# Optimization experiments

Measured on AMD Instinct MI355X. Metric: run time of the kernel, lower is better.

Reference implementation:

```python
import jax, jax.numpy as jnp
import numpy as np

N_NODES = 100000
N_EDGES = 1200000
N_GRAPHS = 1024
IN_DIM, HIDDEN, OUT_DIM = 4, 64, 2
BN_EPS = 1e-5


def setup_inputs() -> dict:
    key = jax.random.key(0)
    ks = jax.random.split(key, 12)
    x = jax.random.normal(ks[0], (N_NODES, IN_DIM), dtype=jnp.float32)
    edge_index = jax.random.randint(ks[1], (2, N_EDGES), 0, N_NODES, dtype=jnp.int64)
    batch = jnp.sort(jax.random.randint(ks[2], (N_NODES,), 0, N_GRAPHS, dtype=jnp.int64))
    s = 1.0 / np.sqrt(HIDDEN)
    return {
        "x": x,
        "edge_index": edge_index,
        "batch": batch,
        "W_enc": jax.random.normal(ks[3], (IN_DIM, HIDDEN), dtype=jnp.float32) * 0.5,
        "b_enc": jnp.zeros((HIDDEN,), dtype=jnp.float32),
        "bn_gamma": jnp.ones((HIDDEN,), dtype=jnp.float32),
        "bn_beta": jnp.zeros((HIDDEN,), dtype=jnp.float32),
        "bn_mean": jax.random.normal(ks[4], (HIDDEN,), dtype=jnp.float32) * 0.1,
        "bn_var": jax.random.uniform(ks[5], (HIDDEN,), dtype=jnp.float32, minval=0.5, maxval=1.5),
        "W_gcn": jax.random.normal(ks[6], (HIDDEN, HIDDEN), dtype=jnp.float32) * s,
        "b_gcn": jnp.zeros((HIDDEN,), dtype=jnp.float32),
        "W_cls1": jax.random.normal(ks[7], (HIDDEN, HIDDEN), dtype=jnp.float32) * s,
        "b_cls1": jnp.zeros((HIDDEN,), dtype=jnp.float32),
        "W_cls2": jax.random.normal(ks[8], (HIDDEN, OUT_DIM), dtype=jnp.float32) * s,
        "b_cls2": jnp.zeros((OUT_DIM,), dtype=jnp.float32),
    }


def reference(x, edge_index, batch, W_enc, b_enc, bn_gamma, bn_beta, bn_mean, bn_var,
              W_gcn, b_gcn, W_cls1, b_cls1, W_cls2, b_cls2):
    n = x.shape[0]
    # Encoder: Linear -> ReLU -> Dropout(eval=identity) -> BatchNorm1d (running stats)
    h = jnp.maximum(x @ W_enc + b_enc, 0.0)
    h = (h - bn_mean) * jax.lax.rsqrt(bn_var + BN_EPS) * bn_gamma + bn_beta
    # GCNConv (PyG): add self-loops, symmetric deg^{-1/2} normalization
    loop = jnp.arange(n, dtype=edge_index.dtype)
    src = jnp.concatenate([edge_index[0], loop])  # [E+N]
    dst = jnp.concatenate([edge_index[1], loop])
    deg = jnp.zeros((n,), dtype=h.dtype).at[dst].add(1.0)
    dis = jnp.where(deg > 0, jax.lax.rsqrt(jnp.maximum(deg, 1.0)), 0.0)
    norm = dis[src] * dis[dst]  # [E+N]
    hw = h @ W_gcn  # [N, H]
    msg = hw[src] * norm[:, None]  # gather + scale, [E+N, H]
    agg = jax.ops.segment_sum(msg, dst, num_segments=n) + b_gcn
    agg = jnp.maximum(agg, 0.0)  # .relu()
    # global_mean_pool over graphs
    sums = jax.ops.segment_sum(agg, batch, num_segments=N_GRAPHS)  # [G, H]
    cnts = jax.ops.segment_sum(jnp.ones((n,), dtype=agg.dtype), batch, num_segments=N_GRAPHS)
    gm = sums / jnp.maximum(cnts, 1.0)[:, None]
    # Classifier: Linear -> ReLU -> Dropout(eval) -> Linear
    out = jnp.maximum(gm @ W_cls1 + b_cls1, 0.0) @ W_cls2 + b_cls2
    return out
```

## Files before the change

### kernel.cpp

```cpp
#include <hip/hip_runtime.h>

#define N_NODES  100000
#define N_EDGES  1200000
#define N_GRAPHS 1024

#define BUCK_SHIFT 10
#define BUCK_NODES 1024
#define NBUCK 98
#define FBLK  512
#define CHUNK ((N_EDGES + FBLK - 1) / FBLK)

__device__ __forceinline__ unsigned short f2bf(float f) {
  unsigned u = __float_as_uint(f);
  return (unsigned short)((u + 0x7fffu + ((u >> 16) & 1u)) >> 16);
}
__device__ __forceinline__ float bf2f(unsigned short b) {
  return __uint_as_float(((unsigned)b) << 16);
}

__global__ __launch_bounds__(256) void k_cnt(const int* __restrict__ ei,
                                             int* __restrict__ cnt,
                                             float* __restrict__ gsum) {
  __shared__ int h[NBUCK];
  int t = threadIdx.x;
  for (int i = t; i < NBUCK; i += 256) h[i] = 0;
  int gi = blockIdx.x * 256 + t;
  if (gi < N_GRAPHS * 64) gsum[gi] = 0.f;
  __syncthreads();
  int start = blockIdx.x * CHUNK, end = min(start + CHUNK, N_EDGES);
  for (int e = start + t; e < end; e += 256)
    atomicAdd(&h[ei[N_EDGES + e] >> BUCK_SHIFT], 1);
  __syncthreads();
  for (int b = t; b < NBUCK; b += 256)
    cnt[b * FBLK + blockIdx.x] = h[b];
}

__global__ __launch_bounds__(256) void k_colscan(int* __restrict__ cnt,
                                                 int* __restrict__ tot) {
  __shared__ int wsum[4];
  int b = blockIdx.x, t = threadIdx.x;
  int v0 = cnt[b * FBLK + 2 * t], v1 = cnt[b * FBLK + 2 * t + 1];
  int a = v0 + v1;
  int lane = t & 63, w = t >> 6;
  int incl = a;
  #pragma unroll
  for (int off = 1; off < 64; off <<= 1) {
    int y = __shfl_up(incl, off);
    if (lane >= off) incl += y;
  }
  if (lane == 63) wsum[w] = incl;
  __syncthreads();
  if (t == 0) {
    int s = 0;
    #pragma unroll
    for (int i = 0; i < 4; ++i) { int x = wsum[i]; wsum[i] = s; s += x; }
    tot[b] = s;
  }
  __syncthreads();
  int excl = wsum[w] + incl - a;
  cnt[b * FBLK + 2 * t] = excl;
  cnt[b * FBLK + 2 * t + 1] = excl + v0;
}

__global__ void k_base(const int* __restrict__ tot, int* __restrict__ base) {
  __shared__ int s[128];
  int t = threadIdx.x;
  int v = (t < NBUCK) ? tot[t] : 0;
  s[t] = v;
  __syncthreads();
  for (int off = 1; off < 128; off <<= 1) {
    int x = (t >= off) ? s[t - off] : 0;
    __syncthreads();
    s[t] += x;
    __syncthreads();
  }
  if (t < NBUCK) base[t] = s[t] - v;
  if (t == 0) base[NBUCK] = N_EDGES;
}

__global__ __launch_bounds__(256) void k_fill(const int* __restrict__ ei,
                                              const int* __restrict__ cnt,
                                              const int* __restrict__ base,
                                              int* __restrict__ binned) {
  __shared__ int cur[NBUCK];
  int t = threadIdx.x, blk = blockIdx.x;
  for (int b = t; b < NBUCK; b += 256) cur[b] = base[b] + cnt[b * FBLK + blk];
  __syncthreads();
  int start = blk * CHUNK, end = min(start + CHUNK, N_EDGES);
  for (int e = start + t; e < end; e += 256) {
    int src = ei[e];
    int dst = ei[N_EDGES + e];
    int b = dst >> BUCK_SHIFT;
    int p = atomicAdd(&cur[b], 1);
    binned[p] = src | ((dst & (BUCK_NODES - 1)) << 17);
  }
}

__global__ __launch_bounds__(1024) void k_csr(const int* __restrict__ base,
                                              const int* __restrict__ binned,
                                              int* __restrict__ csr,
                                              int* __restrict__ row_start,
                                              float* __restrict__ dis) {
  __shared__ int hist[BUCK_NODES];
  __shared__ int wsum[16];
  int t = threadIdx.x;
  int blk = blockIdx.x;
  int b0 = base[blk];
  int nE = base[blk + 1] - b0;
  int node0 = blk << BUCK_SHIFT;
  int nNodes = min(BUCK_NODES, N_NODES - node0);
  hist[t] = 0;
  __syncthreads();
  for (int i = t; i < nE; i += 1024)
    atomicAdd(&hist[(unsigned)binned[b0 + i] >> 17], 1);
  __syncthreads();
  int v = hist[t];
  int lane = t & 63, w = t >> 6;
  int incl = v;
  #pragma unroll
  for (int off = 1; off < 64; off <<= 1) {
    int y = __shfl_up(incl, off);
    if (lane >= off) incl += y;
  }
  if (lane == 63) wsum[w] = incl;
  __syncthreads();
  if (t == 0) {
    int s = 0;
    #pragma unroll
    for (int i = 0; i < 16; ++i) { int x = wsum[i]; wsum[i] = s; s += x; }
  }
  __syncthreads();
  int excl = wsum[w] + incl - v;
  hist[t] = excl;
  if (t < nNodes) {
    row_start[node0 + t] = b0 + excl;
    dis[node0 + t] = rsqrtf((float)(v + 1));
  }
  if (t == 0 && blk == NBUCK - 1) row_start[N_NODES] = N_EDGES;
  __syncthreads();
  for (int i = t; i < nE; i += 1024) {
    int vv = binned[b0 + i];
    int d = (unsigned)vv >> 17;
    int p = atomicAdd(&hist[d], 1);
    csr[b0 + p] = vv & 0x1FFFF;
  }
}

__global__ __launch_bounds__(256) void k_enc(
    const float* __restrict__ x,
    const float* __restrict__ Wenc, const float* __restrict__ benc,
    const float* __restrict__ gamma, const float* __restrict__ beta,
    const float* __restrict__ mean,  const float* __restrict__ var,
    const float* __restrict__ Wgcn,  const float* __restrict__ dis,
    unsigned short* __restrict__ hws) {
  int lane = threadIdx.x & 63;
  int wv = (blockIdx.x * 256 + threadIdx.x) >> 6;
  float be = benc[lane];
  float sc = gamma[lane] * rsqrtf(var[lane] + 1e-5f);
  float mu = mean[lane], bt = beta[lane];
  float w0 = Wenc[lane], w1 = Wenc[64 + lane], w2 = Wenc[128 + lane], w3 = Wenc[192 + lane];
  float wreg[64];
  #pragma unroll
  for (int k = 0; k < 64; ++k) wreg[k] = Wgcn[k * 64 + lane];
  int n0 = wv * 16;
  for (int i = 0; i < 16; ++i) {
    int n = n0 + i;
    float4 xv = ((const float4*)x)[n];
    float h = fmaf(xv.w, w3, fmaf(xv.z, w2, fmaf(xv.y, w1, fmaf(xv.x, w0, be))));
    h = fmaxf(h, 0.f);
    float hbn = (h - mu) * sc + bt;
    int hb = __float_as_int(hbn);
    float a0 = 0.f, a1 = 0.f, a2 = 0.f, a3 = 0.f;
    #pragma unroll
    for (int k = 0; k < 64; k += 4) {
      a0 = fmaf(__int_as_float(__builtin_amdgcn_readlane(hb, k)),     wreg[k],     a0);
      a1 = fmaf(__int_as_float(__builtin_amdgcn_readlane(hb, k + 1)), wreg[k + 1], a1);
      a2 = fmaf(__int_as_float(__builtin_amdgcn_readlane(hb, k + 2)), wreg[k + 2], a2);
      a3 = fmaf(__int_as_float(__builtin_amdgcn_readlane(hb, k + 3)), wreg[k + 3], a3);
    }
    float acc = ((a0 + a1) + (a2 + a3)) * dis[n];
    hws[(size_t)n * 64 + lane] = f2bf(acc);
  }
}

__global__ __launch_bounds__(256) void k_gather(
    const int* __restrict__ row_start, const int* __restrict__ csr,
    const float* __restrict__ dis, const unsigned short* __restrict__ hws,
    const int* __restrict__ batch, const float* __restrict__ bgcn,
    float* __restrict__ gsum) {
  int lane = threadIdx.x & 63;
  int wv = blockIdx.x * 4 + (threadIdx.x >> 6);
  int nb = wv * 4;
  if (nb >= N_NODES) return;
  float bias = bgcn[lane];
  float vout[4];
  int gid[4];
  #pragma unroll
  for (int k = 0; k < 4; ++k) {
    int n = nb + k;
    int st = row_start[n], en = row_start[n + 1];
    float dn = dis[n];
    float a0 = 0.f, a1 = 0.f, a2 = 0.f, a3 = 0.f;
    for (int c = st; c < en; c += 64) {
      int idx = c + lane;
      int sj = (idx < en) ? csr[idx] : 0;
      int m = min(64, en - c);
      int j = 0;
      for (; j + 8 <= m; j += 8) {
        int s0 = __shfl(sj, j),     s1 = __shfl(sj, j + 1);
        int s2 = __shfl(sj, j + 2), s3 = __shfl(sj, j + 3);
        int s4 = __shfl(sj, j + 4), s5 = __shfl(sj, j + 5);
        int s6 = __shfl(sj, j + 6), s7 = __shfl(sj, j + 7);
        float r0 = bf2f(hws[(size_t)s0 * 64 + lane]);
        float r1 = bf2f(hws[(size_t)s1 * 64 + lane]);
        float r2 = bf2f(hws[(size_t)s2 * 64 + lane]);
        float r3 = bf2f(hws[(size_t)s3 * 64 + lane]);
        float r4 = bf2f(hws[(size_t)s4 * 64 + lane]);
        float r5 = bf2f(hws[(size_t)s5 * 64 + lane]);
        float r6 = bf2f(hws[(size_t)s6 * 64 + lane]);
        float r7 = bf2f(hws[(size_t)s7 * 64 + lane]);
        a0 += r0; a1 += r1; a2 += r2; a3 += r3;
        a0 += r4; a1 += r5; a2 += r6; a3 += r7;
      }
      for (; j < m; ++j) {
        int s = __shfl(sj, j);
        a0 += bf2f(hws[(size_t)s * 64 + lane]);
      }
    }
    float self = bf2f(hws[(size_t)n * 64 + lane]);
    vout[k] = fmaxf(dn * (((a0 + a1) + (a2 + a3)) + self) + bias, 0.f);
    gid[k] = batch[n];
  }
  float vs = vout[0];
  int cg = gid[0];
  #pragma unroll
  for (int k = 1; k < 4; ++k) {
    if (gid[k] == cg) vs += vout[k];
    else {
      atomicAdd(&gsum[cg * 64 + lane], vs);
      vs = vout[k]; cg = gid[k];
    }
  }
  atomicAdd(&gsum[cg * 64 + lane], vs);
}

__global__ void k_cls(const float* __restrict__ gsum, const int* __restrict__ batch,
                      const float* __restrict__ W1, const float* __restrict__ b1,
                      const float* __restrict__ W2, const float* __restrict__ b2,
                      float* __restrict__ out) {
  __shared__ float gm[64];
  __shared__ int cntS;
  int j = threadIdx.x;
  int g = blockIdx.x;
  if (j == 0) {
    int lo = 0, hi = N_NODES;
    while (lo < hi) { int mid = (lo + hi) >> 1; if (batch[mid] < g) lo = mid + 1; else hi = mid; }
    int lo2 = lo, hi2 = N_NODES;
    while (lo2 < hi2) { int mid = (lo2 + hi2) >> 1; if (batch[mid] < g + 1) lo2 = mid + 1; else hi2 = mid; }
    cntS = lo2 - lo;
  }
  __syncthreads();
  float denom = fmaxf((float)cntS, 1.0f);
  gm[j] = gsum[g * 64 + j] / denom;
  __syncthreads();
  float hid = b1[j];
  #pragma unroll
  for (int k = 0; k < 64; ++k) hid += gm[k] * W1[k * 64 + j];
  hid = fmaxf(hid, 0.f);
  float o0 = hid * W2[j * 2 + 0];
  float o1 = hid * W2[j * 2 + 1];
  #pragma unroll
  for (int off = 32; off > 0; off >>= 1) {
    o0 += __shfl_down(o0, off);
    o1 += __shfl_down(o1, off);
  }
  if (j == 0) {
    out[g * 2 + 0] = o0 + b2[0];
    out[g * 2 + 1] = o1 + b2[1];
  }
}

extern "C" void kernel_launch(void* const* d_in, const int* in_sizes, int n_in,
                              void* d_out, int out_size, void* d_ws, size_t ws_size,
                              hipStream_t stream) {
  const float* x     = (const float*)d_in[0];
  const int*   ei    = (const int*)d_in[1];
  const int*   batch = (const int*)d_in[2];
  const float* Wenc  = (const float*)d_in[3];
  const float* benc  = (const float*)d_in[4];
  const float* gamma = (const float*)d_in[5];
  const float* beta  = (const float*)d_in[6];
  const float* mean  = (const float*)d_in[7];
  const float* var   = (const float*)d_in[8];
  const float* Wgcn  = (const float*)d_in[9];
  const float* bgcn  = (const float*)d_in[10];
  const float* W1    = (const float*)d_in[11];
  const float* b1    = (const float*)d_in[12];
  const float* W2    = (const float*)d_in[13];
  const float* b2    = (const float*)d_in[14];
  float* out = (float*)d_out;

  char* ws = (char*)d_ws;
  float*          gsum      = (float*)ws;          ws += (size_t)N_GRAPHS * 64 * 4;
  int*            cnt       = (int*)ws;            ws += (size_t)NBUCK * FBLK * 4;
  int*            tot       = (int*)ws;            ws += 128 * 4;
  int*            basep     = (int*)ws;            ws += 128 * 4;
  int*            binned    = (int*)ws;            ws += (size_t)N_EDGES * 4;
  int*            csr       = (int*)ws;            ws += (size_t)N_EDGES * 4;
  int*            row_start = (int*)ws;            ws += (size_t)(N_NODES + 32) * 4;
  float*          dis       = (float*)ws;          ws += (size_t)N_NODES * 4;
  unsigned short* hws       = (unsigned short*)ws; ws += (size_t)N_NODES * 64 * 2;

  k_cnt<<<FBLK, 256, 0, stream>>>(ei, cnt, gsum);
  k_colscan<<<NBUCK, 256, 0, stream>>>(cnt, tot);
  k_base<<<1, 128, 0, stream>>>(tot, basep);
  k_fill<<<FBLK, 256, 0, stream>>>(ei, cnt, basep, binned);
  k_csr<<<NBUCK, 1024, 0, stream>>>(basep, binned, csr, row_start, dis);
  k_enc<<<(N_NODES / 16 + 3) / 4, 256, 0, stream>>>(x, Wenc, benc, gamma, beta, mean, var,
                                                    Wgcn, dis, hws);
  k_gather<<<(N_NODES / 16), 256, 0, stream>>>(row_start, csr, dis, hws, batch, bgcn, gsum);
  k_cls<<<N_GRAPHS, 64, 0, stream>>>(gsum, batch, W1, b1, W2, b2, out);
}
```

Baseline: 200.5 us.

## Fold bucket base scan into fill and CSR kernels; reshape gather launch

```diff
diff --git a/kernel.cpp b/kernel.cpp
--- a/kernel.cpp
+++ b/kernel.cpp
@@ -62,29 +62,20 @@
   cnt[b * FBLK + 2 * t + 1] = excl + v0;
 }
 
-__global__ void k_base(const int* __restrict__ tot, int* __restrict__ base) {
-  __shared__ int s[128];
-  int t = threadIdx.x;
-  int v = (t < NBUCK) ? tot[t] : 0;
-  s[t] = v;
-  __syncthreads();
-  for (int off = 1; off < 128; off <<= 1) {
-    int x = (t >= off) ? s[t - off] : 0;
-    __syncthreads();
-    s[t] += x;
-    __syncthreads();
-  }
-  if (t < NBUCK) base[t] = s[t] - v;
-  if (t == 0) base[NBUCK] = N_EDGES;
-}
-
 __global__ __launch_bounds__(256) void k_fill(const int* __restrict__ ei,
                                               const int* __restrict__ cnt,
-                                              const int* __restrict__ base,
+                                              const int* __restrict__ tot,
                                               int* __restrict__ binned) {
+  __shared__ int totS[NBUCK];
   __shared__ int cur[NBUCK];
   int t = threadIdx.x, blk = blockIdx.x;
-  for (int b = t; b < NBUCK; b += 256) cur[b] = base[b] + cnt[b * FBLK + blk];
+  if (t < NBUCK) totS[t] = tot[t];
+  __syncthreads();
+  if (t < NBUCK) {
+    int s = 0;
+    for (int i = 0; i < t; ++i) s += totS[i];
+    cur[t] = s + cnt[t * FBLK + blk];
+  }
   __syncthreads();
   int start = blk * CHUNK, end = min(start + CHUNK, N_EDGES);
   for (int e = start + t; e < end; e += 256) {
@@ -96,26 +87,38 @@
   }
 }
 
-__global__ __launch_bounds__(1024) void k_csr(const int* __restrict__ base,
+__global__ __launch_bounds__(1024) void k_csr(const int* __restrict__ tot,
                                               const int* __restrict__ binned,
                                               int* __restrict__ csr,
                                               int* __restrict__ row_start,
                                               float* __restrict__ dis) {
   __shared__ int hist[BUCK_NODES];
   __shared__ int wsum[16];
+  __shared__ int b0S;
   int t = threadIdx.x;
   int blk = blockIdx.x;
-  int b0 = base[blk];
-  int nE = base[blk + 1] - b0;
+  int lane = t & 63, w = t >> 6;
+  int pv = (t < blk) ? tot[t] : 0;
+  #pragma unroll
+  for (int off = 32; off > 0; off >>= 1) pv += __shfl_down(pv, off);
+  if (lane == 0) wsum[w] = pv;
+  hist[t] = 0;
+  __syncthreads();
+  if (t == 0) {
+    int s = 0;
+    #pragma unroll
+    for (int i = 0; i < 16; ++i) s += wsum[i];
+    b0S = s;
+  }
+  __syncthreads();
+  int b0 = b0S;
+  int nE = tot[blk];
   int node0 = blk << BUCK_SHIFT;
   int nNodes = min(BUCK_NODES, N_NODES - node0);
-  hist[t] = 0;
-  __syncthreads();
   for (int i = t; i < nE; i += 1024)
     atomicAdd(&hist[(unsigned)binned[b0 + i] >> 17], 1);
   __syncthreads();
   int v = hist[t];
-  int lane = t & 63, w = t >> 6;
   int incl = v;
   #pragma unroll
   for (int off = 1; off < 64; off <<= 1) {
@@ -183,15 +186,13 @@
   }
 }
 
-__global__ __launch_bounds__(256) void k_gather(
+__global__ __launch_bounds__(64) void k_gather(
     const int* __restrict__ row_start, const int* __restrict__ csr,
     const float* __restrict__ dis, const unsigned short* __restrict__ hws,
     const int* __restrict__ batch, const float* __restrict__ bgcn,
     float* __restrict__ gsum) {
-  int lane = threadIdx.x & 63;
-  int wv = blockIdx.x * 4 + (threadIdx.x >> 6);
-  int nb = wv * 4;
-  if (nb >= N_NODES) return;
+  int lane = threadIdx.x;
+  int nb = blockIdx.x * 4;
   float bias = bgcn[lane];
   float vout[4];
   int gid[4];
@@ -202,28 +203,21 @@
     float dn = dis[n];
     float a0 = 0.f, a1 = 0.f, a2 = 0.f, a3 = 0.f;
     for (int c = st; c < en; c += 64) {
-      int idx = c + lane;
-      int sj = (idx < en) ? csr[idx] : 0;
       int m = min(64, en - c);
+      int chunk = (c + lane < en) ? csr[c + lane] : 0;
       int j = 0;
-      for (; j + 8 <= m; j += 8) {
-        int s0 = __shfl(sj, j),     s1 = __shfl(sj, j + 1);
-        int s2 = __shfl(sj, j + 2), s3 = __shfl(sj, j + 3);
-        int s4 = __shfl(sj, j + 4), s5 = __shfl(sj, j + 5);
-        int s6 = __shfl(sj, j + 6), s7 = __shfl(sj, j + 7);
-        float r0 = bf2f(hws[(size_t)s0 * 64 + lane]);
-        float r1 = bf2f(hws[(size_t)s1 * 64 + lane]);
-        float r2 = bf2f(hws[(size_t)s2 * 64 + lane]);
-        float r3 = bf2f(hws[(size_t)s3 * 64 + lane]);
-        float r4 = bf2f(hws[(size_t)s4 * 64 + lane]);
-        float r5 = bf2f(hws[(size_t)s5 * 64 + lane]);
-        float r6 = bf2f(hws[(size_t)s6 * 64 + lane]);
-        float r7 = bf2f(hws[(size_t)s7 * 64 + lane]);
-        a0 += r0; a1 += r1; a2 += r2; a3 += r3;
-        a0 += r4; a1 += r5; a2 += r6; a3 += r7;
+      for (; j + 4 <= m; j += 4) {
+        int s0 = __builtin_amdgcn_readlane(chunk, j);
+        int s1 = __builtin_amdgcn_readlane(chunk, j + 1);
+        int s2 = __builtin_amdgcn_readlane(chunk, j + 2);
+        int s3 = __builtin_amdgcn_readlane(chunk, j + 3);
+        a0 += bf2f(hws[(size_t)s0 * 64 + lane]);
+        a1 += bf2f(hws[(size_t)s1 * 64 + lane]);
+        a2 += bf2f(hws[(size_t)s2 * 64 + lane]);
+        a3 += bf2f(hws[(size_t)s3 * 64 + lane]);
       }
       for (; j < m; ++j) {
-        int s = __shfl(sj, j);
+        int s = __builtin_amdgcn_readlane(chunk, j);
         a0 += bf2f(hws[(size_t)s * 64 + lane]);
       }
     }
@@ -304,7 +298,6 @@
   float*          gsum      = (float*)ws;          ws += (size_t)N_GRAPHS * 64 * 4;
   int*            cnt       = (int*)ws;            ws += (size_t)NBUCK * FBLK * 4;
   int*            tot       = (int*)ws;            ws += 128 * 4;
-  int*            basep     = (int*)ws;            ws += 128 * 4;
   int*            binned    = (int*)ws;            ws += (size_t)N_EDGES * 4;
   int*            csr       = (int*)ws;            ws += (size_t)N_EDGES * 4;
   int*            row_start = (int*)ws;            ws += (size_t)(N_NODES + 32) * 4;
@@ -313,11 +306,10 @@
 
   k_cnt<<<FBLK, 256, 0, stream>>>(ei, cnt, gsum);
   k_colscan<<<NBUCK, 256, 0, stream>>>(cnt, tot);
-  k_base<<<1, 128, 0, stream>>>(tot, basep);
-  k_fill<<<FBLK, 256, 0, stream>>>(ei, cnt, basep, binned);
-  k_csr<<<NBUCK, 1024, 0, stream>>>(basep, binned, csr, row_start, dis);
+  k_fill<<<FBLK, 256, 0, stream>>>(ei, cnt, tot, binned);
+  k_csr<<<NBUCK, 1024, 0, stream>>>(tot, binned, csr, row_start, dis);
   k_enc<<<(N_NODES / 16 + 3) / 4, 256, 0, stream>>>(x, Wenc, benc, gamma, beta, mean, var,
                                                     Wgcn, dis, hws);
-  k_gather<<<(N_NODES / 16), 256, 0, stream>>>(row_start, csr, dis, hws, batch, bgcn, gsum);
+  k_gather<<<(N_NODES / 4), 64, 0, stream>>>(row_start, csr, dis, hws, batch, bgcn, gsum);
   k_cls<<<N_GRAPHS, 64, 0, stream>>>(gsum, batch, W1, b1, W2, b2, out);
 }
```

New measurement: 195.2 us. -2.6%, faster.
